# Optimization experiments

Measured on AMD Instinct MI355X. Metric: run time of the kernel, lower is better.

## Reference

```python
import jax, jax.numpy as jnp
import numpy as np

B, S, D = 2, 2048, 4096
H, HKV, HD = 32, 8, 128
G = H // HKV  # GQA groups
ROPE_BASE = 10000.0


def setup_inputs() -> dict:
    key = jax.random.key(0)
    kx, kq, kk, kv, ko = jax.random.split(key, 5)
    w = 0.02  # init scale for stability
    return {
        "x": jax.random.normal(kx, (B, S, D), dtype=jnp.float32),
        "Wq": jax.random.normal(kq, (D, H * HD), dtype=jnp.float32) * w,
        "Wk": jax.random.normal(kk, (D, HKV * HD), dtype=jnp.float32) * w,
        "Wv": jax.random.normal(kv, (D, HKV * HD), dtype=jnp.float32) * w,
        "Wo": jax.random.normal(ko, (H * HD, D), dtype=jnp.float32) * w,
    }


def _rope(t):
    # t: (B, h, S, HD); rotate-half RoPE, positions = arange(S)
    s = t.shape[2]
    pos = jnp.arange(s, dtype=jnp.float32)
    inv_freq = 1.0 / (ROPE_BASE ** (jnp.arange(0, HD, 2, dtype=jnp.float32) / HD))
    ang = pos[:, None] * inv_freq[None, :]            # (S, HD/2)
    cos = jnp.concatenate([jnp.cos(ang), jnp.cos(ang)], axis=-1)  # (S, HD)
    sin = jnp.concatenate([jnp.sin(ang), jnp.sin(ang)], axis=-1)
    t1, t2 = jnp.split(t, 2, axis=-1)
    rot = jnp.concatenate([-t2, t1], axis=-1)
    return t * cos.astype(t.dtype) + rot * sin.astype(t.dtype)


def reference(x, Wq, Wk, Wv, Wo):
    b, s, _ = x.shape
    q = (x @ Wq).reshape(b, s, H, HD).transpose(0, 2, 1, 3)      # (B,H,S,HD)
    k = (x @ Wk).reshape(b, s, HKV, HD).transpose(0, 2, 1, 3)    # (B,HKV,S,HD)
    v = (x @ Wv).reshape(b, s, HKV, HD).transpose(0, 2, 1, 3)
    q = _rope(q)
    k = _rope(k)
    # GQA: broadcast KV heads across groups instead of repeat_interleave
    qg = q.reshape(b, HKV, G, s, HD)
    scale = 1.0 / jnp.sqrt(jnp.asarray(HD, dtype=x.dtype))
    scores = jnp.einsum('bkgsd,bktd->bkgst', qg, k) * scale       # (B,HKV,G,S,S)
    causal = jnp.tril(jnp.ones((s, s), dtype=bool))
    scores = jnp.where(causal, scores, jnp.finfo(scores.dtype).min)
    p = jax.nn.softmax(scores, axis=-1)
    out = jnp.einsum('bkgst,bktd->bkgsd', p, v)                   # (B,HKV,G,S,HD)
    out = out.reshape(b, H, s, HD).transpose(0, 2, 1, 3).reshape(b, s, H * HD)
    return out @ Wo
```

## Files before the change

kernel.cpp:

```cpp
#include <hip/hip_runtime.h>
#include <hip/hip_bf16.h>

#define B_   2
#define S_   2048
#define D_   4096
#define H_   32
#define HKV_ 8
#define HD_  128
#define QKVS 6144

typedef __bf16 bf16;
typedef __bf16 bf16x8 __attribute__((ext_vector_type(8)));
typedef __bf16 bf16x4 __attribute__((ext_vector_type(4)));
typedef float  f32x4  __attribute__((ext_vector_type(4)));


__global__ void cast_f32_bf16_kernel(const float* __restrict__ in, bf16* __restrict__ out, int n) {
    int i = (blockIdx.x * blockDim.x + threadIdx.x) * 4;
    if (i >= n) return;
    const float4 v = *(const float4*)(in + i);
    bf16x4 o;
    o[0] = (bf16)v.x; o[1] = (bf16)v.y; o[2] = (bf16)v.z; o[3] = (bf16)v.w;
    *(bf16x4*)(out + i) = o;
}

__global__ void transpose_cast_kernel(const float* __restrict__ W, bf16* __restrict__ WT, int K, int N) {
    __shared__ float t[32][33];
    const int n0 = blockIdx.x * 32, k0 = blockIdx.y * 32;
    const int tx = threadIdx.x, ty = threadIdx.y;
    #pragma unroll
    for (int i = ty; i < 32; i += 8) t[i][tx] = W[(size_t)(k0 + i) * N + n0 + tx];
    __syncthreads();
    #pragma unroll
    for (int i = ty; i < 32; i += 8) WT[(size_t)(n0 + i) * K + k0 + tx] = (bf16)t[tx][i];
}

__global__ void transpose_v_kernel(const bf16* __restrict__ V, bf16* __restrict__ Vt) {
    __shared__ bf16 t[32][33];
    const int bh = blockIdx.z;
    const int b = bh >> 3, hk = bh & 7;
    const int d0 = blockIdx.x * 32, s0 = blockIdx.y * 32;
    const int tx = threadIdx.x, ty = threadIdx.y;
    #pragma unroll
    for (int i = ty; i < 32; i += 8)
        t[i][tx] = V[((size_t)(b * S_ + s0 + i)) * QKVS + hk * HD_ + d0 + tx];
    __syncthreads();
    #pragma unroll
    for (int i = ty; i < 32; i += 8)
        Vt[((size_t)(bh * HD_ + d0 + i)) * S_ + s0 + tx] = t[tx][i];
}

__global__ void rope_kernel(bf16* __restrict__ T, int nh, int stride) {
    const int row = blockIdx.x;
    const int pos = row & (S_ - 1);
    const size_t base = (size_t)row * stride;
    const int npairs = nh * 64;
    const float c = 13.287712379549449f / 64.0f;
    for (int p = threadIdx.x; p < npairs; p += blockDim.x) {
        const int h = p >> 6, d = p & 63;
        const float invf = exp2f(-(float)d * c);
        const float ang = (float)pos * invf;
        float sn, cs;
        sincosf(ang, &sn, &cs);
        const size_t i1 = base + (size_t)h * HD_ + d;
        const size_t i2 = i1 + 64;
        const float a  = (float)T[i1];
        const float b2 = (float)T[i2];
        T[i1] = (bf16)(a * cs - b2 * sn);
        T[i2] = (bf16)(b2 * cs + a * sn);
    }
}

__device__ __forceinline__ void gload_lds16(const bf16* g, bf16* l) {
    __builtin_amdgcn_global_load_lds((const __attribute__((address_space(1))) void*)g,
                                     (__attribute__((address_space(3))) void*)l, 16, 0, 0);
}


#define PHASE256(QM, QN, STAGE_STMT, DO_VM)                                              \
    {                                                                                    \
        bf16x8 af[4][2], bfr[2][2];                                                      \
        _Pragma("unroll") for (int i = 0; i < 4; ++i) {                                  \
            const int row = wm * 128 + (QM * 4 + i) * 16 + lr;                           \
            _Pragma("unroll") for (int kk = 0; kk < 2; ++kk)                             \
                af[i][kk] = *(const bf16x8*)(curA + row * 64 + (((kk * 4 + lg) ^ (lr & 7)) << 3)); \
        }                                                                                \
        _Pragma("unroll") for (int i2 = 0; i2 < 2; ++i2) {                               \
            const int row = wn * 64 + (QN * 2 + i2) * 16 + lr;                           \
            _Pragma("unroll") for (int kk = 0; kk < 2; ++kk)                             \
                bfr[i2][kk] = *(const bf16x8*)(curB + row * 64 + (((kk * 4 + lg) ^ (lr & 7)) << 3)); \
        }                                                                                \
        STAGE_STMT;                                                                      \
        if (DO_VM) asm volatile("s_waitcnt vmcnt(4)" ::: "memory");                      \
        __builtin_amdgcn_s_barrier();                                                    \
        asm volatile("s_waitcnt lgkmcnt(0)" ::: "memory");                               \
        __builtin_amdgcn_sched_barrier(0);                                               \
        __builtin_amdgcn_s_setprio(1);                                                   \
        _Pragma("unroll") for (int i = 0; i < 4; ++i)                                    \
            _Pragma("unroll") for (int i2 = 0; i2 < 2; ++i2)                             \
                _Pragma("unroll") for (int kk = 0; kk < 2; ++kk)                         \
                    acc[QM * 4 + i][QN * 2 + i2] = __builtin_amdgcn_mfma_f32_16x16x32_bf16( \
                        af[i][kk], bfr[i2][kk], acc[QM * 4 + i][QN * 2 + i2], 0, 0, 0);  \
        __builtin_amdgcn_s_setprio(0);                                                   \
        __builtin_amdgcn_s_barrier();                                                    \
    }

template <typename CT>
__global__ __launch_bounds__(512, 2) void gemm_bt256_kernel(const bf16* __restrict__ A,
                                                            const bf16* __restrict__ Bm,
                                                            CT* __restrict__ C,
                                                            int M, int N, int K) {
    __shared__ bf16 sm[65536];
    const int nbx = N >> 8;
    const int cpx = gridDim.x >> 3;
    const int bid = blockIdx.x;
    const int swz = (bid & 7) * cpx + (bid >> 3);
    const int m0 = (swz / nbx) << 8;
    const int n0 = (swz % nbx) << 8;

    const int tid = threadIdx.x;
    const int w = tid >> 6, lane = tid & 63;
    const int wm = w >> 2, wn = w & 3;
    const int lg = lane >> 4, lr = lane & 15;
    const int nkt = K >> 6;

    const bf16* Ab = A + (size_t)m0 * K;
    const bf16* Bb = Bm + (size_t)n0 * K;

    const int u8 = tid >> 3;
    const int schunk = ((tid & 7) ^ (u8 & 7)) << 3;

    auto stageA = [&](int buf, int kt, int h) {
        bf16* dst = sm + buf * 32768 + h * 4096 + tid * 8;
        const bf16* src = Ab + (size_t)(h * 64 + u8) * K + kt * 64 + schunk;
        gload_lds16(src, dst);
        gload_lds16(src + (size_t)128 * K, dst + 8192);
    };
    auto stageB = [&](int buf, int kt, int h) {
        bf16* dst = sm + buf * 32768 + 16384 + h * 2048 + ((u8 >> 5) << 12) + ((u8 & 31) << 6) + ((tid & 7) << 3);
        const bf16* src = Bb + (size_t)(h * 32 + ((u8 >> 5) << 6) + (u8 & 31)) * K + kt * 64 + schunk;
        gload_lds16(src, dst);
        gload_lds16(src + (size_t)128 * K, dst + 8192);
    };

    f32x4 acc[8][4] = {};

    stageA(0, 0, 0); stageA(0, 0, 1); stageB(0, 0, 0); stageB(0, 0, 1);
    stageB(1, 1, 0); stageA(1, 1, 0);
    asm volatile("s_waitcnt vmcnt(4)" ::: "memory");
    __builtin_amdgcn_s_barrier();

    for (int t = 0; t < nkt; ++t) {
        const int cur = t & 1;
        const bf16* curA = sm + cur * 32768;
        const bf16* curB = curA + 16384;
        PHASE256(0, 0, { if (t + 1 < nkt) stageA(cur ^ 1, t + 1, 1); }, 0)
        PHASE256(1, 0, { if (t + 1 < nkt) stageB(cur ^ 1, t + 1, 1); }, 0)
        PHASE256(0, 1, { if (t + 2 < nkt) stageB(cur, t + 2, 0); }, 0)
        PHASE256(1, 1, { if (t + 2 < nkt) stageA(cur, t + 2, 0); }, 1)
    }

    #pragma unroll
    for (int mi = 0; mi < 8; ++mi)
        #pragma unroll
        for (int ni = 0; ni < 4; ++ni)
            #pragma unroll
            for (int r = 0; r < 4; ++r) {
                const int row = m0 + wm * 128 + mi * 16 + lg * 4 + r;
                const int col = n0 + wn * 64 + ni * 16 + lr;
                C[(size_t)row * N + col] = (CT)acc[mi][ni][r];
            }
}

#define KVB_ 64

__global__ __launch_bounds__(256) void attn_kernel(const bf16* __restrict__ Q,
                                                   const bf16* __restrict__ Kb,
                                                   const bf16* __restrict__ Vt,
                                                   bf16* __restrict__ O) {
    __shared__ bf16 lds[24576];
    bf16* Ks = lds;
    bf16* Vs = lds + 8192;

    const int flat = blockIdx.x;
    const int x = flat & 7;
    const int j = flat >> 3;
    const int hkb = x * 2 + (j & 1);
    const int qt = 63 - (j >> 1);
    const int hk = hkb & 7, b = hkb >> 3;
    const int q0 = qt * 32;

    const int tid = threadIdx.x;
    const int w = tid >> 6, lane = tid & 63;
    const int lg = lane >> 4, lr = lane & 15;
    const int h = hk * 4 + w;
    bf16* pb = lds + 16384 + w * 2048;

    const bf16* qbase = Q + ((size_t)(b * S_ + q0 + lr)) * QKVS + h * HD_ + lg * 8;
    bf16x8 qf[2][4];
    #pragma unroll
    for (int m = 0; m < 2; m++)
        #pragma unroll
        for (int kk = 0; kk < 4; kk++)
            qf[m][kk] = *(const bf16x8*)(qbase + (size_t)m * 16 * QKVS + kk * 32);

    const bf16* Kh = Kb + ((size_t)b * S_) * QKVS + hk * HD_;
    const bf16* Vh = Vt + ((size_t)(b * HKV_ + hk)) * HD_ * S_;

    const int krow_s  = tid >> 4;
    const int kchnk_s = (tid & 15) ^ (tid >> 4);
    const int vrow_s  = tid >> 3;
    const int vchnk_s = (tid & 7) ^ ((tid >> 3) & 7);

    f32x4 acc[2][8];
    #pragma unroll
    for (int m = 0; m < 2; m++)
        #pragma unroll
        for (int dt = 0; dt < 8; dt++)
            acc[m][dt] = (f32x4){0.f, 0.f, 0.f, 0.f};
    float rowmax[2], rowsum[2];
    #pragma unroll
    for (int m = 0; m < 2; m++) { rowmax[m] = -1e30f; rowsum[m] = 0.f; }

    const float scale = 0.08838834764831845f;
    const int nt = (q0 + 32 + KVB_ - 1) / KVB_;

    for (int it = 0; it < nt; ++it) {
        const int k0 = it * KVB_;
        #pragma unroll
        for (int jj = 0; jj < 4; jj++)
            gload_lds16(Kh + (size_t)(k0 + jj * 16 + krow_s) * QKVS + kchnk_s * 8,
                        Ks + jj * 2048 + tid * 8);
        #pragma unroll
        for (int jj = 0; jj < 4; jj++)
            gload_lds16(Vh + (size_t)(jj * 32 + vrow_s) * S_ + k0 + vchnk_s * 8,
                        Vs + jj * 2048 + tid * 8);
        __syncthreads();

        f32x4 st[2][4];
        #pragma unroll
        for (int m = 0; m < 2; m++)
            #pragma unroll
            for (int kt = 0; kt < 4; kt++)
                st[m][kt] = (f32x4){0.f, 0.f, 0.f, 0.f};
        #pragma unroll
        for (int kt = 0; kt < 4; kt++) {
            bf16x8 kf[4];
            #pragma unroll
            for (int kk = 0; kk < 4; kk++)
                kf[kk] = *(const bf16x8*)(Ks + (kt * 16 + lr) * 128 + (((kk * 4 + lg) ^ lr) << 3));
            #pragma unroll
            for (int m = 0; m < 2; m++)
                #pragma unroll
                for (int kk = 0; kk < 4; kk++)
                    st[m][kt] = __builtin_amdgcn_mfma_f32_16x16x32_bf16(kf[kk], qf[m][kk], st[m][kt], 0, 0, 0);
        }

        const bool need_mask = (k0 + KVB_ - 1 > q0);
        #pragma unroll
        for (int m = 0; m < 2; m++)
            #pragma unroll
            for (int kt = 0; kt < 4; kt++)
                #pragma unroll
                for (int r = 0; r < 4; r++) {
                    float s = st[m][kt][r] * scale;
                    if (need_mask) {
                        const int qg = q0 + m * 16 + lr;
                        const int kg = k0 + kt * 16 + lg * 4 + r;
                        s = (kg <= qg) ? s : -1e30f;
                    }
                    st[m][kt][r] = s;
                }

        float vmax[2];
        #pragma unroll
        for (int m = 0; m < 2; m++) {
            float v = st[m][0][0];
            #pragma unroll
            for (int kt = 0; kt < 4; kt++)
                #pragma unroll
                for (int r = 0; r < 4; r++)
                    v = fmaxf(v, st[m][kt][r]);
            v = fmaxf(v, __shfl_xor(v, 16));
            v = fmaxf(v, __shfl_xor(v, 32));
            vmax[m] = v;
        }
        const bool upd = (vmax[0] > rowmax[0] + 8.0f) || (vmax[1] > rowmax[1] + 8.0f);
        if (__any(upd)) {
            #pragma unroll
            for (int m = 0; m < 2; m++) {
                const float mn = fmaxf(rowmax[m], vmax[m]);
                const float fac = __expf(rowmax[m] - mn);
                rowmax[m] = mn;
                rowsum[m] *= fac;
                #pragma unroll
                for (int r = 0; r < 4; r++) {
                    const float facr = __shfl(fac, lg * 4 + r);
                    #pragma unroll
                    for (int dt = 0; dt < 8; dt++)
                        acc[m][dt][r] *= facr;
                }
            }
        }
        #pragma unroll
        for (int m = 0; m < 2; m++) {
            float ssum = 0.f;
            #pragma unroll
            for (int kt = 0; kt < 4; kt++)
                #pragma unroll
                for (int r = 0; r < 4; r++) {
                    const float pv = __expf(st[m][kt][r] - rowmax[m]);
                    st[m][kt][r] = pv;
                    ssum += pv;
                }
            ssum += __shfl_xor(ssum, 16);
            ssum += __shfl_xor(ssum, 32);
            rowsum[m] += ssum;
        }

        #pragma unroll
        for (int m = 0; m < 2; m++) {
            const int qrow = m * 16 + lr;
            #pragma unroll
            for (int kt = 0; kt < 4; kt++)
                #pragma unroll
                for (int r = 0; r < 4; r++)
                    pb[(qrow * 64 + kt * 16 + lg * 4 + r) ^ ((qrow & 7) << 3)] = (bf16)st[m][kt][r];
        }

        bf16x8 pf[2][2];
        #pragma unroll
        for (int m = 0; m < 2; m++)
            #pragma unroll
            for (int ks = 0; ks < 2; ks++)
                pf[m][ks] = *(const bf16x8*)(pb + (m * 16 + lr) * 64 + ((ks * 32 + lg * 8) ^ ((lr & 7) << 3)));
        #pragma unroll
        for (int dt = 0; dt < 8; dt++) {
            bf16x8 vf[2];
            #pragma unroll
            for (int ks = 0; ks < 2; ks++)
                vf[ks] = *(const bf16x8*)(Vs + (dt * 16 + lr) * 64 + (((ks * 4 + lg) ^ (lr & 7)) << 3));
            #pragma unroll
            for (int m = 0; m < 2; m++)
                #pragma unroll
                for (int ks = 0; ks < 2; ks++)
                    acc[m][dt] = __builtin_amdgcn_mfma_f32_16x16x32_bf16(pf[m][ks], vf[ks], acc[m][dt], 0, 0, 0);
        }
        __syncthreads();
    }

    #pragma unroll
    for (int m = 0; m < 2; m++) {
        float inv[4];
        #pragma unroll
        for (int r = 0; r < 4; r++)
            inv[r] = 1.0f / __shfl(rowsum[m], lg * 4 + r);
        #pragma unroll
        for (int dt = 0; dt < 8; dt++)
            #pragma unroll
            for (int r = 0; r < 4; r++) {
                const size_t row = (size_t)(b * S_ + q0 + m * 16 + lg * 4 + r);
                O[row * (H_ * HD_) + h * HD_ + dt * 16 + lr] = (bf16)(acc[m][dt][r] * inv[r]);
            }
    }
}


extern "C" void kernel_launch(void* const* d_in, const int* in_sizes, int n_in,
                              void* d_out, int out_size, void* d_ws, size_t ws_size,
                              hipStream_t stream) {
    const float* x  = (const float*)d_in[0];
    const float* Wq = (const float*)d_in[1];
    const float* Wk = (const float*)d_in[2];
    const float* Wv = (const float*)d_in[3];
    const float* Wo = (const float*)d_in[4];
    float* out = (float*)d_out;

    const size_t NX   = (size_t)B_ * S_ * D_;
    const size_t NQKVW= (size_t)QKVS * D_;
    const size_t NQKV = (size_t)B_ * S_ * QKVS;
    const size_t NWK  = (size_t)D_ * HKV_ * HD_;

    bf16* p = (bf16*)d_ws;
    bf16* xb    = p;  p += NX;
    bf16* WqkvT = p;  p += NQKVW;
    bf16* QKV   = p;  p += NQKV;
    bf16* Ab  = xb;
    bf16* Vtb = WqkvT;
    bf16* WoT = WqkvT + NWK;

    cast_f32_bf16_kernel<<<(int)(NX / 1024), 256, 0, stream>>>(x, xb, (int)NX);
    transpose_cast_kernel<<<dim3((H_ * HD_) / 32, D_ / 32), dim3(32, 8), 0, stream>>>(Wq, WqkvT, D_, H_ * HD_);
    transpose_cast_kernel<<<dim3((HKV_ * HD_) / 32, D_ / 32), dim3(32, 8), 0, stream>>>(Wk, WqkvT + (size_t)(H_ * HD_) * D_, D_, HKV_ * HD_);
    transpose_cast_kernel<<<dim3((HKV_ * HD_) / 32, D_ / 32), dim3(32, 8), 0, stream>>>(Wv, WqkvT + (size_t)(H_ * HD_ + HKV_ * HD_) * D_, D_, HKV_ * HD_);

    gemm_bt256_kernel<bf16><<<384, 512, 0, stream>>>(xb, WqkvT, QKV, B_ * S_, QKVS, D_);

    rope_kernel<<<B_ * S_, 256, 0, stream>>>(QKV, H_, QKVS);
    rope_kernel<<<B_ * S_, 256, 0, stream>>>(QKV + H_ * HD_, HKV_, QKVS);

    transpose_v_kernel<<<dim3(HD_ / 32, S_ / 32, B_ * HKV_), dim3(32, 8), 0, stream>>>(QKV + H_ * HD_ + HKV_ * HD_, Vtb);

    attn_kernel<<<1024, 256, 0, stream>>>(QKV, QKV + H_ * HD_, Vtb, Ab);

    transpose_cast_kernel<<<dim3(D_ / 32, (H_ * HD_) / 32), dim3(32, 8), 0, stream>>>(Wo, WoT, H_ * HD_, D_);
    gemm_bt256_kernel<float><<<256, 512, 0, stream>>>(Ab, WoT, out, B_ * S_, D_, H_ * HD_);
}
```

Measured before the change: 659.1 us.

## Split QKV GEMM into Q and KV launches; reorder 256-tile pipeline with register reuse

The fused QKV projection GEMM becomes two launches. The 256x256 pipelined kernel now computes only the Q part (256 blocks), and a new simple 128x128 single-buffered GEMM computes the K/V columns. An output-stride parameter is added so each launch can write into the shared QKV buffer. The 256 kernel's main loop is also restructured: the A fragment is kept in registers across two phases and two B fragment sets are reused, which cuts redundant LDS reads, and an explicit vmcnt(0) is added on the last iteration. The likely aim is a better block count per CU. The risk is that the KV part runs on a much less efficient kernel with no double buffering.

Measured after the change: 604.1 us. -8.3%, faster.

```diff
diff --git a/kernel.cpp b/kernel.cpp
--- a/kernel.cpp
+++ b/kernel.cpp
@@ -77,39 +77,58 @@
 }
 
 
-#define PHASE256(QM, QN, STAGE_STMT, DO_VM)                                              \
-    {                                                                                    \
-        bf16x8 af[4][2], bfr[2][2];                                                      \
-        _Pragma("unroll") for (int i = 0; i < 4; ++i) {                                  \
-            const int row = wm * 128 + (QM * 4 + i) * 16 + lr;                           \
-            _Pragma("unroll") for (int kk = 0; kk < 2; ++kk)                             \
-                af[i][kk] = *(const bf16x8*)(curA + row * 64 + (((kk * 4 + lg) ^ (lr & 7)) << 3)); \
-        }                                                                                \
-        _Pragma("unroll") for (int i2 = 0; i2 < 2; ++i2) {                               \
-            const int row = wn * 64 + (QN * 2 + i2) * 16 + lr;                           \
-            _Pragma("unroll") for (int kk = 0; kk < 2; ++kk)                             \
-                bfr[i2][kk] = *(const bf16x8*)(curB + row * 64 + (((kk * 4 + lg) ^ (lr & 7)) << 3)); \
-        }                                                                                \
-        STAGE_STMT;                                                                      \
-        if (DO_VM) asm volatile("s_waitcnt vmcnt(4)" ::: "memory");                      \
-        __builtin_amdgcn_s_barrier();                                                    \
-        asm volatile("s_waitcnt lgkmcnt(0)" ::: "memory");                               \
-        __builtin_amdgcn_sched_barrier(0);                                               \
-        __builtin_amdgcn_s_setprio(1);                                                   \
-        _Pragma("unroll") for (int i = 0; i < 4; ++i)                                    \
-            _Pragma("unroll") for (int i2 = 0; i2 < 2; ++i2)                             \
-                _Pragma("unroll") for (int kk = 0; kk < 2; ++kk)                         \
-                    acc[QM * 4 + i][QN * 2 + i2] = __builtin_amdgcn_mfma_f32_16x16x32_bf16( \
-                        af[i][kk], bfr[i2][kk], acc[QM * 4 + i][QN * 2 + i2], 0, 0, 0);  \
-        __builtin_amdgcn_s_setprio(0);                                                   \
-        __builtin_amdgcn_s_barrier();                                                    \
+template <typename CT>
+__global__ __launch_bounds__(256) void gemm_bt_kernel(const bf16* __restrict__ A,
+                                                      const bf16* __restrict__ Bm,
+                                                      CT* __restrict__ C,
+                                                      int M, int Cs, int K) {
+    __shared__ bf16 As[128 * 32];
+    __shared__ bf16 Bs[128 * 32];
+    const int m0 = blockIdx.x * 128, n0 = blockIdx.y * 128;
+    const int tid = threadIdx.x;
+    const int lane = tid & 63, wid = tid >> 6;
+    const int wm = wid >> 1, wn = wid & 1;
+    const int lg = lane >> 4, lr = lane & 15;
+    f32x4 acc[4][4] = {};
+    const int arow = tid >> 2;
+    const int achunk = (tid & 3) * 8;
+    for (int k0 = 0; k0 < K; k0 += 32) {
+        gload_lds16(A  + (size_t)(m0 + arow) * K      + k0 + achunk, As + tid * 8);
+        gload_lds16(A  + (size_t)(m0 + 64 + arow) * K + k0 + achunk, As + 2048 + tid * 8);
+        gload_lds16(Bm + (size_t)(n0 + arow) * K      + k0 + achunk, Bs + tid * 8);
+        gload_lds16(Bm + (size_t)(n0 + 64 + arow) * K + k0 + achunk, Bs + 2048 + tid * 8);
+        __syncthreads();
+        bf16x8 af[4], bfv[4];
+        #pragma unroll
+        for (int i = 0; i < 4; i++) {
+            af[i]  = *(const bf16x8*)(As + (wm * 64 + i * 16 + lr) * 32 + lg * 8);
+            bfv[i] = *(const bf16x8*)(Bs + (wn * 64 + i * 16 + lr) * 32 + lg * 8);
+        }
+        #pragma unroll
+        for (int mi = 0; mi < 4; mi++)
+            #pragma unroll
+            for (int ni = 0; ni < 4; ni++)
+                acc[mi][ni] = __builtin_amdgcn_mfma_f32_16x16x32_bf16(af[mi], bfv[ni], acc[mi][ni], 0, 0, 0);
+        __syncthreads();
     }
+    #pragma unroll
+    for (int mi = 0; mi < 4; mi++)
+        #pragma unroll
+        for (int ni = 0; ni < 4; ni++)
+            #pragma unroll
+            for (int r = 0; r < 4; r++) {
+                const int row = m0 + wm * 64 + mi * 16 + lg * 4 + r;
+                const int col = n0 + wn * 64 + ni * 16 + lr;
+                C[(size_t)row * Cs + col] = (CT)acc[mi][ni][r];
+            }
+}
+
 
 template <typename CT>
 __global__ __launch_bounds__(512, 2) void gemm_bt256_kernel(const bf16* __restrict__ A,
                                                             const bf16* __restrict__ Bm,
                                                             CT* __restrict__ C,
-                                                            int M, int N, int K) {
+                                                            int M, int N, int K, int Cs) {
     __shared__ bf16 sm[65536];
     const int nbx = N >> 8;
     const int cpx = gridDim.x >> 3;
@@ -150,15 +169,75 @@
     asm volatile("s_waitcnt vmcnt(4)" ::: "memory");
     __builtin_amdgcn_s_barrier();
 
+    #define MFMA_Q(MI0, NI0, AREG, BREG)                                                     \
+        __builtin_amdgcn_s_setprio(1);                                                       \
+        _Pragma("unroll") for (int i = 0; i < 4; ++i)                                        \
+            _Pragma("unroll") for (int i2 = 0; i2 < 2; ++i2)                                 \
+                _Pragma("unroll") for (int kk = 0; kk < 2; ++kk)                             \
+                    acc[MI0 + i][NI0 + i2] = __builtin_amdgcn_mfma_f32_16x16x32_bf16(        \
+                        AREG[i][kk], BREG[i2][kk], acc[MI0 + i][NI0 + i2], 0, 0, 0);         \
+        __builtin_amdgcn_s_setprio(0);                                                       \
+        __builtin_amdgcn_s_barrier();
+
+    #define SYNC_IN()                                                                        \
+        __builtin_amdgcn_s_barrier();                                                        \
+        asm volatile("s_waitcnt lgkmcnt(0)" ::: "memory");                                   \
+        __builtin_amdgcn_sched_barrier(0);
+
     for (int t = 0; t < nkt; ++t) {
         const int cur = t & 1;
         const bf16* curA = sm + cur * 32768;
         const bf16* curB = curA + 16384;
-        PHASE256(0, 0, { if (t + 1 < nkt) stageA(cur ^ 1, t + 1, 1); }, 0)
-        PHASE256(1, 0, { if (t + 1 < nkt) stageB(cur ^ 1, t + 1, 1); }, 0)
-        PHASE256(0, 1, { if (t + 2 < nkt) stageB(cur, t + 2, 0); }, 0)
-        PHASE256(1, 1, { if (t + 2 < nkt) stageA(cur, t + 2, 0); }, 1)
+        bf16x8 afc[4][2], b0[2][2], b1[2][2];
+
+        #pragma unroll
+        for (int i = 0; i < 4; ++i) {
+            const int row = wm * 128 + i * 16 + lr;
+            #pragma unroll
+            for (int kk = 0; kk < 2; ++kk)
+                afc[i][kk] = *(const bf16x8*)(curA + row * 64 + (((kk * 4 + lg) ^ (lr & 7)) << 3));
+        }
+        #pragma unroll
+        for (int i2 = 0; i2 < 2; ++i2) {
+            const int row = wn * 64 + i2 * 16 + lr;
+            #pragma unroll
+            for (int kk = 0; kk < 2; ++kk)
+                b0[i2][kk] = *(const bf16x8*)(curB + row * 64 + (((kk * 4 + lg) ^ (lr & 7)) << 3));
+        }
+        if (t + 1 < nkt) stageA(cur ^ 1, t + 1, 1);
+        if (t + 1 == nkt) asm volatile("s_waitcnt vmcnt(0)" ::: "memory");
+        SYNC_IN()
+        MFMA_Q(0, 0, afc, b0)
+
+        #pragma unroll
+        for (int i2 = 0; i2 < 2; ++i2) {
+            const int row = wn * 64 + (2 + i2) * 16 + lr;
+            #pragma unroll
+            for (int kk = 0; kk < 2; ++kk)
+                b1[i2][kk] = *(const bf16x8*)(curB + row * 64 + (((kk * 4 + lg) ^ (lr & 7)) << 3));
+        }
+        if (t + 1 < nkt) stageB(cur ^ 1, t + 1, 1);
+        SYNC_IN()
+        MFMA_Q(0, 2, afc, b1)
+
+        #pragma unroll
+        for (int i = 0; i < 4; ++i) {
+            const int row = wm * 128 + (4 + i) * 16 + lr;
+            #pragma unroll
+            for (int kk = 0; kk < 2; ++kk)
+                afc[i][kk] = *(const bf16x8*)(curA + row * 64 + (((kk * 4 + lg) ^ (lr & 7)) << 3));
+        }
+        if (t + 2 < nkt) stageB(cur, t + 2, 0);
+        SYNC_IN()
+        MFMA_Q(4, 0, afc, b0)
+
+        if (t + 2 < nkt) stageA(cur, t + 2, 0);
+        asm volatile("s_waitcnt vmcnt(4)" ::: "memory");
+        SYNC_IN()
+        MFMA_Q(4, 2, afc, b1)
     }
+    #undef MFMA_Q
+    #undef SYNC_IN
 
     #pragma unroll
     for (int mi = 0; mi < 8; ++mi)
@@ -168,7 +247,7 @@
             for (int r = 0; r < 4; ++r) {
                 const int row = m0 + wm * 128 + mi * 16 + lg * 4 + r;
                 const int col = n0 + wn * 64 + ni * 16 + lr;
-                C[(size_t)row * N + col] = (CT)acc[mi][ni][r];
+                C[(size_t)row * Cs + col] = (CT)acc[mi][ni][r];
             }
 }
 
@@ -394,7 +473,9 @@
     transpose_cast_kernel<<<dim3((HKV_ * HD_) / 32, D_ / 32), dim3(32, 8), 0, stream>>>(Wk, WqkvT + (size_t)(H_ * HD_) * D_, D_, HKV_ * HD_);
     transpose_cast_kernel<<<dim3((HKV_ * HD_) / 32, D_ / 32), dim3(32, 8), 0, stream>>>(Wv, WqkvT + (size_t)(H_ * HD_ + HKV_ * HD_) * D_, D_, HKV_ * HD_);
 
-    gemm_bt256_kernel<bf16><<<384, 512, 0, stream>>>(xb, WqkvT, QKV, B_ * S_, QKVS, D_);
+    gemm_bt256_kernel<bf16><<<256, 512, 0, stream>>>(xb, WqkvT, QKV, B_ * S_, H_ * HD_, D_, QKVS);
+    gemm_bt_kernel<bf16><<<dim3(32, 16), 256, 0, stream>>>(xb, WqkvT + (size_t)(H_ * HD_) * D_,
+                                                           QKV + H_ * HD_, B_ * S_, QKVS, D_);
 
     rope_kernel<<<B_ * S_, 256, 0, stream>>>(QKV, H_, QKVS);
     rope_kernel<<<B_ * S_, 256, 0, stream>>>(QKV + H_ * HD_, HKV_, QKVS);
@@ -404,5 +485,5 @@
     attn_kernel<<<1024, 256, 0, stream>>>(QKV, QKV + H_ * HD_, Vtb, Ab);
 
     transpose_cast_kernel<<<dim3(D_ / 32, (H_ * HD_) / 32), dim3(32, 8), 0, stream>>>(Wo, WoT, H_ * HD_, D_);
-    gemm_bt256_kernel<float><<<256, 512, 0, stream>>>(Ab, WoT, out, B_ * S_, D_, H_ * HD_);
-}
+    gemm_bt256_kernel<float><<<256, 512, 0, stream>>>(Ab, WoT, out, B_ * S_, D_, H_ * HD_, D_);
+}
```
